# Performance work log

Measured on AMD Instinct MI355X. Metric: run time of the kernel, lower is better.

Reference implementation:

```python
import jax, jax.numpy as jnp
import numpy as np

SCALING = 128.0 / 64.0   # alpha / r
DT = 0.1
TAU_MIN = 0.1
TAU_MAX = 10.0
ADAPT_STEPS = 3


def setup_inputs() -> dict:
    key = jax.random.key(0)
    ks = jax.random.split(key, 6)
    B, S, D, O, R = 4, 4096, 4096, 4096, 64
    x = jax.random.normal(ks[0], (B, S, D), dtype=jnp.float32)
    # kaiming_uniform-ish init for lora_A; lora_B nominally zeros in torch but
    # we use small random values so the dynamics/matmul are non-trivial.
    lora_A = jax.random.normal(ks[1], (R, D), dtype=jnp.float32) * (1.0 / np.sqrt(D))
    lora_B = jax.random.normal(ks[2], (O, R), dtype=jnp.float32) * 0.02
    hidden_B = jnp.zeros((O, R), dtype=jnp.float32)
    W_gate = jax.random.normal(ks[3], (R, 2 * R), dtype=jnp.float32) * (1.0 / np.sqrt(2 * R))
    b_gate = jnp.zeros((R,), dtype=jnp.float32)
    W_tau = jax.random.normal(ks[4], (R, 2 * R), dtype=jnp.float32) * (1.0 / np.sqrt(2 * R))
    b_tau = jnp.zeros((R,), dtype=jnp.float32)
    return {"x": x, "lora_A": lora_A, "lora_B": lora_B, "hidden_B": hidden_B,
            "W_gate": W_gate, "b_gate": b_gate, "W_tau": W_tau, "b_tau": b_tau}


def _liquid_step(h, target, W_gate, b_gate, W_tau, b_tau):
    # Batched over all out_features rows at once: h, target are [O, r].
    inp = jnp.concatenate([target, h], axis=-1)               # [O, 2r]
    f = jax.nn.sigmoid(inp @ W_gate.T + b_gate)               # gate f(x, B, t)
    tau = TAU_MIN + (TAU_MAX - TAU_MIN) * jax.nn.sigmoid(inp @ W_tau.T + b_tau)
    a = 1.0 / tau + f                                         # effective decay rate
    decay = jnp.exp(-a * DT)
    # closed-form integration of dh/dt = -a*h + f*target over dt
    return h * decay + (f / a) * target * (1.0 - decay)


def reference(x, lora_A, lora_B, hidden_B, W_gate, b_gate, W_tau, b_tau):
    # Liquid dynamics update (torch runs this under no_grad on a buffer).
    target = lora_B                                           # [O, r]
    def body(_, h):
        return _liquid_step(h, target, W_gate, b_gate, W_tau, b_tau)
    hidden_new = jax.lax.fori_loop(0, ADAPT_STEPS, body, hidden_B)
    hidden_new = jax.lax.stop_gradient(hidden_new)
    # straight-through: value from liquid state, gradient from lora_B
    B_eff = hidden_new + lora_B - jax.lax.stop_gradient(lora_B)  # [O, r]
    # (B_eff @ lora_A @ x^T)^T == x @ A^T @ B_eff^T
    lora_out = jnp.einsum('bsi,ri,or->bso', x, lora_A, B_eff, optimize=True)
    return lora_out * SCALING
```

## Files before the change

kernel.cpp:

```cpp
#include <hip/hip_runtime.h>


typedef __attribute__((ext_vector_type(8))) short short8;
typedef __attribute__((ext_vector_type(4))) short short4_t;
typedef __attribute__((ext_vector_type(4))) float f32x4;

static __device__ __forceinline__ unsigned short f2bf(float f) {
    unsigned int x;
    __builtin_memcpy(&x, &f, 4);
    x += 0x7fffu + ((x >> 16) & 1);
    return (unsigned short)(x >> 16);
}
static __device__ __forceinline__ float bf2f(unsigned short u) {
    unsigned int x = ((unsigned int)u) << 16;
    float f;
    __builtin_memcpy(&f, &x, 4);
    return f;
}

__global__ __launch_bounds__(256) void liquid_kernel(
    const float* __restrict__ loraB,
    const float* __restrict__ hiddenB,
    const float* __restrict__ Wg,
    const float* __restrict__ bg,
    const float* __restrict__ Wt,
    const float* __restrict__ bt,
    const float* __restrict__ loraA,
    unsigned short* __restrict__ beff,
    unsigned short* __restrict__ abf)
{
    {
        const int idx = (blockIdx.x * 256 + threadIdx.x) * 4;
        f32x4 a = *(const f32x4*)&loraA[idx];
        short4_t ab;
#pragma unroll
        for (int j = 0; j < 4; ++j) ab[j] = (short)f2bf(a[j]);
        *(short4_t*)&abf[idx] = ab;
    }

    __shared__ __align__(16) float inp[16][132];
    const int tid = threadIdx.x;
    const int row = tid >> 4;
    const int cg  = tid & 15;
    const int orow = blockIdx.x * 16 + row;
    const int c0 = cg * 4;

    float tgt[4], h[4], bgv[4], btv[4];
#pragma unroll
    for (int i = 0; i < 4; ++i) {
        tgt[i] = loraB[orow * 64 + c0 + i];
        h[i]   = hiddenB[orow * 64 + c0 + i];
        bgv[i] = bg[c0 + i];
        btv[i] = bt[c0 + i];
        inp[row][c0 + i] = tgt[i];
    }
    for (int step = 0; step < 3; ++step) {
#pragma unroll
        for (int i = 0; i < 4; ++i) inp[row][64 + c0 + i] = h[i];
        __syncthreads();
        float dg[4], dt_[4];
#pragma unroll
        for (int c = 0; c < 4; ++c) { dg[c] = bgv[c]; dt_[c] = btv[c]; }
        for (int k = 0; k < 128; k += 4) {
            f32x4 iv = *(f32x4*)&inp[row][k];
#pragma unroll
            for (int c = 0; c < 4; ++c) {
                f32x4 wgv = *(const f32x4*)&Wg[(c0 + c) * 128 + k];
                f32x4 wtv = *(const f32x4*)&Wt[(c0 + c) * 128 + k];
                dg[c]  += iv[0]*wgv[0] + iv[1]*wgv[1] + iv[2]*wgv[2] + iv[3]*wgv[3];
                dt_[c] += iv[0]*wtv[0] + iv[1]*wtv[1] + iv[2]*wtv[2] + iv[3]*wtv[3];
            }
        }
#pragma unroll
        for (int c = 0; c < 4; ++c) {
            float f   = 1.f / (1.f + __expf(-dg[c]));
            float tau = 0.1f + 9.9f / (1.f + __expf(-dt_[c]));
            float a   = 1.f / tau + f;
            float dec = __expf(-a * 0.1f);
            h[c] = h[c] * dec + (f / a) * tgt[c] * (1.f - dec);
        }
        __syncthreads();
    }
#pragma unroll
    for (int i = 0; i < 4; ++i)
        beff[orow * 64 + c0 + i] = f2bf(h[i]);
}

__global__ __launch_bounds__(512, 4) void lora_gemm_kernel(
    const float* __restrict__ x,
    const unsigned short* __restrict__ abf,
    const unsigned short* __restrict__ beff,
    float* __restrict__ out)
{
    __shared__ __align__(16) union {
        struct { unsigned short xs[32 * 136]; unsigned short as[64 * 136]; } p1;
        struct { unsigned short bs[128 * 72]; float bounce[32 * 132]; } p2;
    } sm;
    __shared__ __align__(16) unsigned short tsh[32 * 72];
    __shared__ __align__(16) unsigned short tsl[32 * 72];

    const int tid  = threadIdx.x;
    const int lane = tid & 63;
    const int w    = tid >> 6;
    const int q    = lane >> 4;
    const int ln   = lane & 15;
    const int m0   = blockIdx.x * 32;
    const int ms   = (w >> 2) * 16;
    const int nc   = (w & 3) * 16;

    const int xr0 = tid >> 5,        xc0 = (tid & 31) * 4;
    const int xr1 = xr0 + 16;
    const int ar0 = tid >> 4,        ac0 = (tid & 15) * 8;
    const int ar1 = ar0 + 32;
    const int br0 = tid >> 3,        bc0 = (tid & 7) * 8;
    const int br1 = br0 + 64;

    f32x4 acc = (f32x4){0.f, 0.f, 0.f, 0.f};

    const float* xp0 = &x[(size_t)(m0 + xr0) * 4096 + xc0];
    const float* xp1 = &x[(size_t)(m0 + xr1) * 4096 + xc0];
    const unsigned short* ap0 = &abf[(size_t)ar0 * 4096 + ac0];
    const unsigned short* ap1 = &abf[(size_t)ar1 * 4096 + ac0];

    f32x4 xcur[2]; short8 acur[2];
    xcur[0] = *(const f32x4*)xp0;
    xcur[1] = *(const f32x4*)xp1;
    acur[0] = *(const short8*)ap0;
    acur[1] = *(const short8*)ap1;

    for (int it = 0; it < 32; ++it) {
        f32x4 xn[2]; short8 an[2];
        if (it < 31) {
            const int k = (it + 1) * 128;
            xn[0] = *(const f32x4*)(xp0 + k);
            xn[1] = *(const f32x4*)(xp1 + k);
            an[0] = *(const short8*)(ap0 + k);
            an[1] = *(const short8*)(ap1 + k);
        }
        __syncthreads();
        {
            short4_t xb0, xb1;
#pragma unroll
            for (int j = 0; j < 4; ++j) {
                xb0[j] = (short)f2bf(xcur[0][j]);
                xb1[j] = (short)f2bf(xcur[1][j]);
            }
            *(short4_t*)&sm.p1.xs[xr0 * 136 + xc0] = xb0;
            *(short4_t*)&sm.p1.xs[xr1 * 136 + xc0] = xb1;
            *(short8*)&sm.p1.as[ar0 * 136 + ac0] = acur[0];
            *(short8*)&sm.p1.as[ar1 * 136 + ac0] = acur[1];
        }
        __syncthreads();
#pragma unroll
        for (int kk = 0; kk < 128; kk += 32) {
            short8 af  = *(short8*)&sm.p1.xs[(ms + ln) * 136 + kk + q * 8];
            short8 bfv = *(short8*)&sm.p1.as[(nc + ln) * 136 + kk + q * 8];
            acc = __builtin_amdgcn_mfma_f32_16x16x32_bf16(af, bfv, acc, 0, 0, 0);
        }
        if (it < 31) {
            xcur[0] = xn[0]; xcur[1] = xn[1];
            acur[0] = an[0]; acur[1] = an[1];
        }
    }
#pragma unroll
    for (int r = 0; r < 4; ++r) {
        float v = acc[r];
        unsigned short hh = f2bf(v);
        tsh[(ms + q * 4 + r) * 72 + nc + ln] = hh;
        tsl[(ms + q * 4 + r) * 72 + nc + ln] = f2bf(v - bf2f(hh));
    }

    const int oc = (w & 3) * 32;
    const unsigned short* bp0 = &beff[(size_t)br0 * 64 + bc0];
    const unsigned short* bp1 = &beff[(size_t)br1 * 64 + bc0];
    short8 bcur[2];
    bcur[0] = *(const short8*)bp0;
    bcur[1] = *(const short8*)bp1;

    for (int it = 0; it < 32; ++it) {
        const int o0 = it * 128;
        short8 bn[2];
        if (it < 31) {
            bn[0] = *(const short8*)(bp0 + (it + 1) * 8192);
            bn[1] = *(const short8*)(bp1 + (it + 1) * 8192);
        }
        __syncthreads();
        *(short8*)&sm.p2.bs[br0 * 72 + bc0] = bcur[0];
        *(short8*)&sm.p2.bs[br1 * 72 + bc0] = bcur[1];
        __syncthreads();
        f32x4 a2[2];
        a2[0] = (f32x4){0.f, 0.f, 0.f, 0.f};
        a2[1] = (f32x4){0.f, 0.f, 0.f, 0.f};
#pragma unroll
        for (int kk = 0; kk < 64; kk += 32) {
            short8 ah = *(short8*)&tsh[(ms + ln) * 72 + kk + q * 8];
            short8 al = *(short8*)&tsl[(ms + ln) * 72 + kk + q * 8];
#pragma unroll
            for (int t = 0; t < 2; ++t) {
                short8 bfv = *(short8*)&sm.p2.bs[(oc + t * 16 + ln) * 72 + kk + q * 8];
                a2[t] = __builtin_amdgcn_mfma_f32_16x16x32_bf16(ah, bfv, a2[t], 0, 0, 0);
                a2[t] = __builtin_amdgcn_mfma_f32_16x16x32_bf16(al, bfv, a2[t], 0, 0, 0);
            }
        }
#pragma unroll
        for (int t = 0; t < 2; ++t)
#pragma unroll
            for (int r = 0; r < 4; ++r)
                sm.p2.bounce[(ms + q * 4 + r) * 132 + oc + t * 16 + ln] =
                    a2[t][r] * 2.0f;
        __syncthreads();
        *(f32x4*)&out[(size_t)(m0 + xr0) * 4096 + o0 + xc0] =
            *(f32x4*)&sm.p2.bounce[xr0 * 132 + xc0];
        *(f32x4*)&out[(size_t)(m0 + xr1) * 4096 + o0 + xc0] =
            *(f32x4*)&sm.p2.bounce[xr1 * 132 + xc0];
        if (it < 31) { bcur[0] = bn[0]; bcur[1] = bn[1]; }
    }
}

extern "C" void kernel_launch(void* const* d_in, const int* in_sizes, int n_in,
                              void* d_out, int out_size, void* d_ws, size_t ws_size,
                              hipStream_t stream) {
    const float* x       = (const float*)d_in[0];
    const float* loraA   = (const float*)d_in[1];
    const float* loraB   = (const float*)d_in[2];
    const float* hiddenB = (const float*)d_in[3];
    const float* Wg      = (const float*)d_in[4];
    const float* bg      = (const float*)d_in[5];
    const float* Wt      = (const float*)d_in[6];
    const float* bt      = (const float*)d_in[7];
    float* out = (float*)d_out;
    unsigned short* beff = (unsigned short*)d_ws;
    unsigned short* abf  = beff + 4096 * 64;

    hipLaunchKernelGGL(liquid_kernel, dim3(256), dim3(256), 0, stream,
                       loraB, hiddenB, Wg, bg, Wt, bt, loraA, beff, abf);
    hipLaunchKernelGGL(lora_gemm_kernel, dim3(512), dim3(512), 0, stream,
                       x, abf, beff, out);
}
```

Before: 562.9 us.

## Shrink GEMM tile to 16 rows and load A and B_eff fragments directly to registers

The fused LoRA GEMM block now covers 16 rows with 256 threads instead of 32 rows with 512, doubling the grid to 1024 blocks. The A and B_eff operands are loaded straight from global memory into MFMA fragments, which drops their LDS staging and most barriers in the second phase. Output is written directly from the accumulators as scattered 4-byte stores instead of going through an LDS bounce buffer for 16-byte coalesced stores. The trade-off is less coalesced output writes on a large fp32 output, plus more redundant A and B_eff reads per block.

New measurement: 616.5 us. 1.1x slower.

```diff
diff --git a/kernel.cpp b/kernel.cpp
--- a/kernel.cpp
+++ b/kernel.cpp
@@ -86,134 +86,110 @@
         beff[orow * 64 + c0 + i] = f2bf(h[i]);
 }
 
-__global__ __launch_bounds__(512, 4) void lora_gemm_kernel(
+__global__ __launch_bounds__(256, 4) void lora_gemm_kernel(
     const float* __restrict__ x,
     const unsigned short* __restrict__ abf,
     const unsigned short* __restrict__ beff,
     float* __restrict__ out)
 {
-    __shared__ __align__(16) union {
-        struct { unsigned short xs[32 * 136]; unsigned short as[64 * 136]; } p1;
-        struct { unsigned short bs[128 * 72]; float bounce[32 * 132]; } p2;
-    } sm;
-    __shared__ __align__(16) unsigned short tsh[32 * 72];
-    __shared__ __align__(16) unsigned short tsl[32 * 72];
+    __shared__ __align__(16) unsigned short xs[16 * 136];
+    __shared__ __align__(16) unsigned short tsh[16 * 72];
+    __shared__ __align__(16) unsigned short tsl[16 * 72];
 
     const int tid  = threadIdx.x;
     const int lane = tid & 63;
     const int w    = tid >> 6;
     const int q    = lane >> 4;
     const int ln   = lane & 15;
-    const int m0   = blockIdx.x * 32;
-    const int ms   = (w >> 2) * 16;
-    const int nc   = (w & 3) * 16;
-
-    const int xr0 = tid >> 5,        xc0 = (tid & 31) * 4;
-    const int xr1 = xr0 + 16;
-    const int ar0 = tid >> 4,        ac0 = (tid & 15) * 8;
-    const int ar1 = ar0 + 32;
-    const int br0 = tid >> 3,        bc0 = (tid & 7) * 8;
-    const int br1 = br0 + 64;
+    const int m0   = blockIdx.x * 16;
+
+    const int sr = tid >> 5;
+    const int sc = (tid & 31) * 4;
+
+    const int nrow = w * 16 + ln;
+    const float* xp0 = &x[(size_t)(m0 + sr) * 4096 + sc];
+    const float* xp1 = &x[(size_t)(m0 + sr + 8) * 4096 + sc];
+    const unsigned short* ap = &abf[(size_t)nrow * 4096 + q * 8];
+
+    f32x4 xc0 = *(const f32x4*)xp0;
+    f32x4 xc1 = *(const f32x4*)xp1;
+    short8 ac[4];
+#pragma unroll
+    for (int kk = 0; kk < 4; ++kk) ac[kk] = *(const short8*)(ap + kk * 32);
 
     f32x4 acc = (f32x4){0.f, 0.f, 0.f, 0.f};
 
-    const float* xp0 = &x[(size_t)(m0 + xr0) * 4096 + xc0];
-    const float* xp1 = &x[(size_t)(m0 + xr1) * 4096 + xc0];
-    const unsigned short* ap0 = &abf[(size_t)ar0 * 4096 + ac0];
-    const unsigned short* ap1 = &abf[(size_t)ar1 * 4096 + ac0];
-
-    f32x4 xcur[2]; short8 acur[2];
-    xcur[0] = *(const f32x4*)xp0;
-    xcur[1] = *(const f32x4*)xp1;
-    acur[0] = *(const short8*)ap0;
-    acur[1] = *(const short8*)ap1;
-
     for (int it = 0; it < 32; ++it) {
-        f32x4 xn[2]; short8 an[2];
+        f32x4 xn0, xn1; short8 an[4];
         if (it < 31) {
             const int k = (it + 1) * 128;
-            xn[0] = *(const f32x4*)(xp0 + k);
-            xn[1] = *(const f32x4*)(xp1 + k);
-            an[0] = *(const short8*)(ap0 + k);
-            an[1] = *(const short8*)(ap1 + k);
+            xn0 = *(const f32x4*)(xp0 + k);
+            xn1 = *(const f32x4*)(xp1 + k);
+#pragma unroll
+            for (int kk = 0; kk < 4; ++kk)
+                an[kk] = *(const short8*)(ap + k + kk * 32);
         }
         __syncthreads();
         {
-            short4_t xb0, xb1;
+            short4_t b0, b1;
 #pragma unroll
             for (int j = 0; j < 4; ++j) {
-                xb0[j] = (short)f2bf(xcur[0][j]);
-                xb1[j] = (short)f2bf(xcur[1][j]);
+                b0[j] = (short)f2bf(xc0[j]);
+                b1[j] = (short)f2bf(xc1[j]);
             }
-            *(short4_t*)&sm.p1.xs[xr0 * 136 + xc0] = xb0;
-            *(short4_t*)&sm.p1.xs[xr1 * 136 + xc0] = xb1;
-            *(short8*)&sm.p1.as[ar0 * 136 + ac0] = acur[0];
-            *(short8*)&sm.p1.as[ar1 * 136 + ac0] = acur[1];
-        }
-        __syncthreads();
-#pragma unroll
-        for (int kk = 0; kk < 128; kk += 32) {
-            short8 af  = *(short8*)&sm.p1.xs[(ms + ln) * 136 + kk + q * 8];
-            short8 bfv = *(short8*)&sm.p1.as[(nc + ln) * 136 + kk + q * 8];
-            acc = __builtin_amdgcn_mfma_f32_16x16x32_bf16(af, bfv, acc, 0, 0, 0);
+            *(short4_t*)&xs[sr * 136 + sc]       = b0;
+            *(short4_t*)&xs[(sr + 8) * 136 + sc] = b1;
+        }
+        __syncthreads();
+#pragma unroll
+        for (int kk = 0; kk < 4; ++kk) {
+            short8 xf = *(short8*)&xs[ln * 136 + kk * 32 + q * 8];
+            acc = __builtin_amdgcn_mfma_f32_16x16x32_bf16(xf, ac[kk], acc, 0, 0, 0);
         }
         if (it < 31) {
-            xcur[0] = xn[0]; xcur[1] = xn[1];
-            acur[0] = an[0]; acur[1] = an[1];
-        }
-    }
+            xc0 = xn0; xc1 = xn1;
+#pragma unroll
+            for (int kk = 0; kk < 4; ++kk) ac[kk] = an[kk];
+        }
+    }
+
 #pragma unroll
     for (int r = 0; r < 4; ++r) {
         float v = acc[r];
         unsigned short hh = f2bf(v);
-        tsh[(ms + q * 4 + r) * 72 + nc + ln] = hh;
-        tsl[(ms + q * 4 + r) * 72 + nc + ln] = f2bf(v - bf2f(hh));
-    }
-
-    const int oc = (w & 3) * 32;
-    const unsigned short* bp0 = &beff[(size_t)br0 * 64 + bc0];
-    const unsigned short* bp1 = &beff[(size_t)br1 * 64 + bc0];
-    short8 bcur[2];
-    bcur[0] = *(const short8*)bp0;
-    bcur[1] = *(const short8*)bp1;
-
-    for (int it = 0; it < 32; ++it) {
-        const int o0 = it * 128;
-        short8 bn[2];
-        if (it < 31) {
-            bn[0] = *(const short8*)(bp0 + (it + 1) * 8192);
-            bn[1] = *(const short8*)(bp1 + (it + 1) * 8192);
-        }
-        __syncthreads();
-        *(short8*)&sm.p2.bs[br0 * 72 + bc0] = bcur[0];
-        *(short8*)&sm.p2.bs[br1 * 72 + bc0] = bcur[1];
-        __syncthreads();
-        f32x4 a2[2];
-        a2[0] = (f32x4){0.f, 0.f, 0.f, 0.f};
-        a2[1] = (f32x4){0.f, 0.f, 0.f, 0.f};
-#pragma unroll
-        for (int kk = 0; kk < 64; kk += 32) {
-            short8 ah = *(short8*)&tsh[(ms + ln) * 72 + kk + q * 8];
-            short8 al = *(short8*)&tsl[(ms + ln) * 72 + kk + q * 8];
-#pragma unroll
-            for (int t = 0; t < 2; ++t) {
-                short8 bfv = *(short8*)&sm.p2.bs[(oc + t * 16 + ln) * 72 + kk + q * 8];
-                a2[t] = __builtin_amdgcn_mfma_f32_16x16x32_bf16(ah, bfv, a2[t], 0, 0, 0);
-                a2[t] = __builtin_amdgcn_mfma_f32_16x16x32_bf16(al, bfv, a2[t], 0, 0, 0);
-            }
-        }
-#pragma unroll
-        for (int t = 0; t < 2; ++t)
-#pragma unroll
-            for (int r = 0; r < 4; ++r)
-                sm.p2.bounce[(ms + q * 4 + r) * 132 + oc + t * 16 + ln] =
-                    a2[t][r] * 2.0f;
-        __syncthreads();
-        *(f32x4*)&out[(size_t)(m0 + xr0) * 4096 + o0 + xc0] =
-            *(f32x4*)&sm.p2.bounce[xr0 * 132 + xc0];
-        *(f32x4*)&out[(size_t)(m0 + xr1) * 4096 + o0 + xc0] =
-            *(f32x4*)&sm.p2.bounce[xr1 * 132 + xc0];
-        if (it < 31) { bcur[0] = bn[0]; bcur[1] = bn[1]; }
+        tsh[(q * 4 + r) * 72 + w * 16 + ln] = hh;
+        tsl[(q * 4 + r) * 72 + w * 16 + ln] = f2bf(v - bf2f(hh));
+    }
+    __syncthreads();
+
+    short8 ah0 = *(short8*)&tsh[ln * 72 + q * 8];
+    short8 ah1 = *(short8*)&tsh[ln * 72 + 32 + q * 8];
+    short8 al0 = *(short8*)&tsl[ln * 72 + q * 8];
+    short8 al1 = *(short8*)&tsl[ln * 72 + 32 + q * 8];
+
+    const int oc = w * 16;
+    const unsigned short* bp = &beff[(size_t)(oc + ln) * 64 + q * 8];
+    const size_t orow0 = (size_t)(m0 + q * 4) * 4096 + oc + ln;
+
+    short8 bc0 = *(const short8*)bp;
+    short8 bc1 = *(const short8*)(bp + 32);
+
+    for (int it = 0; it < 64; ++it) {
+        short8 bn0, bn1;
+        if (it < 63) {
+            bn0 = *(const short8*)(bp + (size_t)(it + 1) * 4096);
+            bn1 = *(const short8*)(bp + (size_t)(it + 1) * 4096 + 32);
+        }
+        f32x4 a2 = (f32x4){0.f, 0.f, 0.f, 0.f};
+        a2 = __builtin_amdgcn_mfma_f32_16x16x32_bf16(ah0, bc0, a2, 0, 0, 0);
+        a2 = __builtin_amdgcn_mfma_f32_16x16x32_bf16(al0, bc0, a2, 0, 0, 0);
+        a2 = __builtin_amdgcn_mfma_f32_16x16x32_bf16(ah1, bc1, a2, 0, 0, 0);
+        a2 = __builtin_amdgcn_mfma_f32_16x16x32_bf16(al1, bc1, a2, 0, 0, 0);
+        const int o0 = it * 64;
+#pragma unroll
+        for (int r = 0; r < 4; ++r)
+            out[orow0 + (size_t)r * 4096 + o0] = a2[r] * 2.0f;
+        if (it < 63) { bc0 = bn0; bc1 = bn1; }
     }
 }
 
@@ -234,6 +210,6 @@
 
     hipLaunchKernelGGL(liquid_kernel, dim3(256), dim3(256), 0, stream,
                        loraB, hiddenB, Wg, bg, Wt, bt, loraA, beff, abf);
-    hipLaunchKernelGGL(lora_gemm_kernel, dim3(512), dim3(512), 0, stream,
+    hipLaunchKernelGGL(lora_gemm_kernel, dim3(1024), dim3(256), 0, stream,
                        x, abf, beff, out);
 }
```
